# Kernel tuning notes

Hardware: AMD Instinct MI355X
Metric: run time of the kernel (lower is better)

## Reference

```python
import jax, jax.numpy as jnp
import numpy as np

N_NODES = 50000
N_EDGES = 100000
NUM_RELS = 200
IN_DIM = 64
OUT_DIM = 64


def setup_inputs() -> dict:
    key = jax.random.key(0)
    k1, k2, k3, k4, k5, k6 = jax.random.split(key, 6)
    input_h = jax.random.normal(k1, (N_NODES, IN_DIM), dtype=jnp.float32)
    src = jax.random.randint(k2, (N_EDGES,), 0, N_NODES, dtype=jnp.int32)
    rel = jax.random.randint(k3, (N_EDGES,), 0, NUM_RELS, dtype=jnp.int32)
    dst = jax.random.randint(k4, (N_EDGES,), 0, N_NODES, dtype=jnp.int32)
    edges = jnp.stack([src, rel, dst], axis=1)  # (E, 3)
    # xavier_normal for relation weight: std = sqrt(2/(in+out))
    w_std = float(np.sqrt(2.0 / (IN_DIM + OUT_DIM)))
    weight = jax.random.normal(k5, (NUM_RELS, IN_DIM, OUT_DIM), dtype=jnp.float32) * w_std
    # xavier_uniform with leaky_relu(0.2) gain for self-loop weight
    gain = float(np.sqrt(2.0 / (1.0 + 0.2 ** 2)))
    bound = gain * float(np.sqrt(6.0 / (IN_DIM + OUT_DIM)))
    self_loop_weight = jax.random.uniform(
        k6, (IN_DIM, OUT_DIM), dtype=jnp.float32, minval=-bound, maxval=bound)
    return {"input_h": input_h, "edges": edges, "weight": weight,
            "self_loop_weight": self_loop_weight}


def reference(input_h, edges, weight, self_loop_weight):
    src, rel, dst = edges[:, 0], edges[:, 1], edges[:, 2]
    num_nodes = input_h.shape[0]
    num_edges = edges.shape[0]

    src_h = input_h[src]                      # (E, in) gather
    w_e = weight[rel]                         # (E, in, out) per-edge weight materialization
    msg = jnp.einsum('ei,eio->eo', src_h, w_e)  # per-edge bmm

    # torch quirk: index_matrix[dst] = arange(E) keeps the LAST write per dst,
    # so each edge's message is replaced by the message of the last edge
    # (in edge order) with the same destination.
    last_idx = jax.ops.segment_max(jnp.arange(num_edges, dtype=jnp.int32), dst,
                                   num_segments=num_nodes)  # (N,)
    msg = msg[last_idx[dst]]                  # (E, out)

    # scatter-mean aggregation by destination (nodes with no in-edges get 0)
    msg_sum = jax.ops.segment_sum(msg, dst, num_segments=num_nodes)          # (N, out)
    count = jax.ops.segment_sum(jnp.ones((num_edges,), msg.dtype), dst,
                                num_segments=num_nodes)                      # (N,)
    agg = jnp.where(count[:, None] > 0, msg_sum / jnp.maximum(count, 1.0)[:, None], 0.0)

    out = input_h @ self_loop_weight + agg    # self-loop plus aggregated messages
    return out
```

## Files before the change

kernel.cpp:

```cpp
#include <hip/hip_runtime.h>

#define N_NODES 50000
#define N_EDGES 100000
#define NUM_RELS 200
#define DIM 64
#define CAP 512
#define TILES 8
#define HPAD 68

#define OFF_LAST 0
#define OFF_CUR  50000
#define OFF_BN   50200
#define OFF_BS   (50200 + NUM_RELS * CAP)

#define BUCKET_BLKS 196
#define SELF_BLKS   782

__global__ void init_kernel(int* __restrict__ ws) {
    int i = blockIdx.x * 256 + threadIdx.x;
    if (i < N_NODES) ws[OFF_LAST + i] = -1;
    if (i < NUM_RELS) ws[OFF_CUR + i] = 0;
}

__global__ void edge_max_kernel(const int* __restrict__ edges, int* __restrict__ ws) {
    int e = blockIdx.x * 256 + threadIdx.x;
    if (e < N_EDGES) atomicMax(&ws[OFF_LAST + edges[e * 3 + 2]], e);
}

__device__ __forceinline__ void gemm44(const float* __restrict__ Hl,
                                       const float* __restrict__ Wl,
                                       int e4, int c4, float acc[4][4]) {
#pragma unroll 8
    for (int k = 0; k < DIM; ++k) {
        float4 hv = *(const float4*)&Hl[k * HPAD + e4 * 4];
        float4 wv = *(const float4*)&Wl[k * DIM + c4 * 4];
        float hvv[4] = {hv.x, hv.y, hv.z, hv.w};
        float wvv[4] = {wv.x, wv.y, wv.z, wv.w};
#pragma unroll
        for (int i = 0; i < 4; ++i)
#pragma unroll
            for (int j = 0; j < 4; ++j)
                acc[i][j] = fmaf(hvv[i], wvv[j], acc[i][j]);
    }
}

__global__ __launch_bounds__(256) void bucket_self_kernel(
    const float* __restrict__ h,
    const int* __restrict__ edges,
    const float* __restrict__ wself,
    int* __restrict__ ws,
    float* __restrict__ out)
{
    __shared__ float Wl[DIM * DIM];
    __shared__ float Hl[DIM * HPAD];

    if (blockIdx.x < BUCKET_BLKS) {
        int n = blockIdx.x * 256 + threadIdx.x;
        if (n < N_NODES) {
            int li = ws[OFF_LAST + n];
            if (li >= 0) {
                int r = edges[li * 3 + 1];
                int s = edges[li * 3 + 0];
                int pos = atomicAdd(&ws[OFF_CUR + r], 1);
                if (pos < CAP) {
                    ws[OFF_BN + r * CAP + pos] = n;
                    ws[OFF_BS + r * CAP + pos] = s;
                }
            }
        }
        return;
    }

    int tile = blockIdx.x - BUCKET_BLKS;
    int base = tile * 64;
    int t = threadIdx.x;

    {
        const float4* wg = (const float4*)wself;
        float4* wl4 = (float4*)Wl;
#pragma unroll
        for (int j = 0; j < 4; ++j) wl4[t + j * 256] = wg[t + j * 256];
    }
    {
        int e = t & 63, q = t >> 6;
        int n = base + e; if (n >= N_NODES) n = N_NODES - 1;
        const float* hp = h + (size_t)n * DIM + q * 16;
#pragma unroll
        for (int j = 0; j < 4; ++j) {
            float4 v = *(const float4*)(hp + j * 4);
            int k0 = q * 16 + j * 4;
            Hl[(k0 + 0) * HPAD + e] = v.x;
            Hl[(k0 + 1) * HPAD + e] = v.y;
            Hl[(k0 + 2) * HPAD + e] = v.z;
            Hl[(k0 + 3) * HPAD + e] = v.w;
        }
    }
    __syncthreads();

    int c4 = t & 15, e4 = t >> 4;
    float acc[4][4];
#pragma unroll
    for (int i = 0; i < 4; ++i)
#pragma unroll
        for (int j = 0; j < 4; ++j) acc[i][j] = 0.f;

    gemm44(Hl, Wl, e4, c4, acc);

#pragma unroll
    for (int i = 0; i < 4; ++i) {
        int n = base + e4 * 4 + i;
        if (n < N_NODES)
            *(float4*)(out + (size_t)n * DIM + c4 * 4) =
                make_float4(acc[i][0], acc[i][1], acc[i][2], acc[i][3]);
    }
}

__global__ __launch_bounds__(256) void msg_kernel(const float* __restrict__ h,
                                                  const float* __restrict__ weight,
                                                  const int* __restrict__ ws,
                                                  float* __restrict__ out) {
    __shared__ float Wl[DIM * DIM];
    __shared__ float Hl[DIM * HPAD];

    int rel  = blockIdx.x >> 3;
    int tile = blockIdx.x & 7;
    int c = ws[OFF_CUR + rel];
    if (c > CAP) c = CAP;
    int start = tile * 64;
    if (start >= c) return;

    int t = threadIdx.x;
    const int* bn = ws + OFF_BN + rel * CAP;
    const int* bs = ws + OFF_BS + rel * CAP;

    {
        const float4* wg = (const float4*)(weight + (size_t)rel * DIM * DIM);
        float4* wl4 = (float4*)Wl;
#pragma unroll
        for (int j = 0; j < 4; ++j) wl4[t + j * 256] = wg[t + j * 256];
    }
    {
        int e = t & 63, q = t >> 6;
        int pos = start + e; if (pos >= c) pos = c - 1;
        int s = bs[pos];
        const float* hp = h + (size_t)s * DIM + q * 16;
#pragma unroll
        for (int j = 0; j < 4; ++j) {
            float4 v = *(const float4*)(hp + j * 4);
            int k0 = q * 16 + j * 4;
            Hl[(k0 + 0) * HPAD + e] = v.x;
            Hl[(k0 + 1) * HPAD + e] = v.y;
            Hl[(k0 + 2) * HPAD + e] = v.z;
            Hl[(k0 + 3) * HPAD + e] = v.w;
        }
    }
    __syncthreads();

    int c4 = t & 15, e4 = t >> 4;
    float acc[4][4];
#pragma unroll
    for (int i = 0; i < 4; ++i)
#pragma unroll
        for (int j = 0; j < 4; ++j) acc[i][j] = 0.f;

    gemm44(Hl, Wl, e4, c4, acc);

#pragma unroll
    for (int i = 0; i < 4; ++i) {
        int pos = start + e4 * 4 + i;
        if (pos < c) {
            int n = bn[pos];
            float* op = out + (size_t)n * DIM + c4 * 4;
            float4 cur = *(const float4*)op;
            *(float4*)op = make_float4(cur.x + acc[i][0], cur.y + acc[i][1],
                                       cur.z + acc[i][2], cur.w + acc[i][3]);
        }
    }
}

extern "C" void kernel_launch(void* const* d_in, const int* in_sizes, int n_in,
                              void* d_out, int out_size, void* d_ws, size_t ws_size,
                              hipStream_t stream) {
    const float* h      = (const float*)d_in[0];
    const int*   edges  = (const int*)d_in[1];
    const float* weight = (const float*)d_in[2];
    const float* wself  = (const float*)d_in[3];
    float* out = (float*)d_out;
    int* ws = (int*)d_ws;

    init_kernel<<<(N_NODES + 255) / 256, 256, 0, stream>>>(ws);
    edge_max_kernel<<<(N_EDGES + 255) / 256, 256, 0, stream>>>(edges, ws);
    bucket_self_kernel<<<BUCKET_BLKS + SELF_BLKS, 256, 0, stream>>>(h, edges, wself, ws, out);
    msg_kernel<<<NUM_RELS * TILES, 256, 0, stream>>>(h, weight, ws, out);
}
```

Measured before the change: 68.78 us.

## Convert inputs to bf16 and use MFMA for self-loop and message GEMMs

Adds a prep kernel that converts node features and relation and self-loop weights to bf16, with the weights transposed, and folds workspace initialization into the same launch. The self-loop and per-relation message GEMMs now use bf16 MFMA 16x16x32 instructions instead of scalar FP32 FMA register tiles. This is meant to cut gather bandwidth and ALU time in exchange for an extra conversion pass over all of h and the weights, plus reduced precision. Outputs are written as scalar stores per lane rather than float4.

After: 59.78 us. 13.1% less time.

```diff
diff --git a/kernel.cpp b/kernel.cpp
--- a/kernel.cpp
+++ b/kernel.cpp
@@ -6,20 +6,74 @@
 #define DIM 64
 #define CAP 512
 #define TILES 8
-#define HPAD 68
+#define KPAD 72
+
+typedef __attribute__((ext_vector_type(8))) short bf16x8;
+typedef __attribute__((ext_vector_type(8))) unsigned short u16x8;
+typedef __attribute__((ext_vector_type(4))) float f32x4;
 
 #define OFF_LAST 0
 #define OFF_CUR  50000
 #define OFF_BN   50200
-#define OFF_BS   (50200 + NUM_RELS * CAP)
-
-#define BUCKET_BLKS 196
-#define SELF_BLKS   782
-
-__global__ void init_kernel(int* __restrict__ ws) {
-    int i = blockIdx.x * 256 + threadIdx.x;
-    if (i < N_NODES) ws[OFF_LAST + i] = -1;
-    if (i < NUM_RELS) ws[OFF_CUR + i] = 0;
+#define OFF_BS   152600
+#define HB_OFF   1020032u
+#define WT_OFF   7420032u
+
+__device__ __forceinline__ unsigned short f2bf(float x) {
+    union { float f; unsigned u; } v; v.f = x;
+    unsigned r = v.u + 0x7FFFu + ((v.u >> 16) & 1u);
+    return (unsigned short)(r >> 16);
+}
+
+#define PREP_INIT 197
+#define PREP_WT   201
+#define PREP_HB   782
+
+__global__ __launch_bounds__(256) void prep_kernel(
+    const float* __restrict__ h, const float* __restrict__ weight,
+    const float* __restrict__ wself, int* __restrict__ ws,
+    unsigned short* __restrict__ hb, unsigned short* __restrict__ wt)
+{
+    __shared__ float Wl[DIM * DIM];
+    int b = blockIdx.x, t = threadIdx.x;
+
+    if (b < PREP_INIT) {
+        int i = b * 256 + t;
+        if (i < N_NODES) ws[OFF_LAST + i] = -1;
+        if (i < NUM_RELS) ws[OFF_CUR + i] = 0;
+        return;
+    }
+    if (b < PREP_INIT + PREP_WT) {
+        int rel = b - PREP_INIT;
+        const float* src = (rel < NUM_RELS) ? (weight + (size_t)rel * DIM * DIM) : wself;
+#pragma unroll
+        for (int j = 0; j < 16; ++j) Wl[t + j * 256] = src[t + j * 256];
+        __syncthreads();
+        int c = t >> 2, q = t & 3;
+        unsigned short tmp[16];
+#pragma unroll
+        for (int kk = 0; kk < 16; ++kk)
+            tmp[kk] = f2bf(Wl[(q * 16 + kk) * DIM + c]);
+        unsigned short* dst = wt + (size_t)rel * DIM * DIM + c * DIM + q * 16;
+        *(u16x8*)dst       = *(const u16x8*)&tmp[0];
+        *(u16x8*)(dst + 8) = *(const u16x8*)&tmp[8];
+        return;
+    }
+    {
+        long off = (long)(b - PREP_INIT - PREP_WT) * 4096 + (long)t * 16;
+        if (off < (long)N_NODES * DIM) {
+            const float4* src = (const float4*)(h + off);
+            unsigned short tmp[16];
+#pragma unroll
+            for (int j = 0; j < 4; ++j) {
+                float4 v = src[j];
+                tmp[j*4+0]=f2bf(v.x); tmp[j*4+1]=f2bf(v.y);
+                tmp[j*4+2]=f2bf(v.z); tmp[j*4+3]=f2bf(v.w);
+            }
+            *(u16x8*)(hb + off)     = *(const u16x8*)&tmp[0];
+            *(u16x8*)(hb + off + 8) = *(const u16x8*)&tmp[8];
+        }
+    }
 }
 
 __global__ void edge_max_kernel(const int* __restrict__ edges, int* __restrict__ ws) {
@@ -27,35 +81,20 @@
     if (e < N_EDGES) atomicMax(&ws[OFF_LAST + edges[e * 3 + 2]], e);
 }
 
-__device__ __forceinline__ void gemm44(const float* __restrict__ Hl,
-                                       const float* __restrict__ Wl,
-                                       int e4, int c4, float acc[4][4]) {
-#pragma unroll 8
-    for (int k = 0; k < DIM; ++k) {
-        float4 hv = *(const float4*)&Hl[k * HPAD + e4 * 4];
-        float4 wv = *(const float4*)&Wl[k * DIM + c4 * 4];
-        float hvv[4] = {hv.x, hv.y, hv.z, hv.w};
-        float wvv[4] = {wv.x, wv.y, wv.z, wv.w};
-#pragma unroll
-        for (int i = 0; i < 4; ++i)
-#pragma unroll
-            for (int j = 0; j < 4; ++j)
-                acc[i][j] = fmaf(hvv[i], wvv[j], acc[i][j]);
-    }
-}
+#define BUCKET_BLKS 196
+#define NODE_TILES 782
 
 __global__ __launch_bounds__(256) void bucket_self_kernel(
-    const float* __restrict__ h,
-    const int* __restrict__ edges,
-    const float* __restrict__ wself,
-    int* __restrict__ ws,
+    const int* __restrict__ edges, const unsigned short* __restrict__ hb,
+    const unsigned short* __restrict__ wt, int* __restrict__ ws,
     float* __restrict__ out)
 {
-    __shared__ float Wl[DIM * DIM];
-    __shared__ float Hl[DIM * HPAD];
+    __shared__ unsigned short Wsh[DIM * KPAD];
+    __shared__ unsigned short Hs[DIM * KPAD];
+    int t = threadIdx.x;
 
     if (blockIdx.x < BUCKET_BLKS) {
-        int n = blockIdx.x * 256 + threadIdx.x;
+        int n = blockIdx.x * 256 + t;
         if (n < N_NODES) {
             int li = ws[OFF_LAST + n];
             if (li >= 0) {
@@ -71,58 +110,54 @@
         return;
     }
 
-    int tile = blockIdx.x - BUCKET_BLKS;
-    int base = tile * 64;
-    int t = threadIdx.x;
-
+    int base = (blockIdx.x - BUCKET_BLKS) * 64;
+    int row = t >> 2, q = t & 3;
     {
-        const float4* wg = (const float4*)wself;
-        float4* wl4 = (float4*)Wl;
-#pragma unroll
-        for (int j = 0; j < 4; ++j) wl4[t + j * 256] = wg[t + j * 256];
-    }
-    {
-        int e = t & 63, q = t >> 6;
-        int n = base + e; if (n >= N_NODES) n = N_NODES - 1;
-        const float* hp = h + (size_t)n * DIM + q * 16;
-#pragma unroll
-        for (int j = 0; j < 4; ++j) {
-            float4 v = *(const float4*)(hp + j * 4);
-            int k0 = q * 16 + j * 4;
-            Hl[(k0 + 0) * HPAD + e] = v.x;
-            Hl[(k0 + 1) * HPAD + e] = v.y;
-            Hl[(k0 + 2) * HPAD + e] = v.z;
-            Hl[(k0 + 3) * HPAD + e] = v.w;
-        }
+        const unsigned short* wsrc = wt + (size_t)NUM_RELS * DIM * DIM + row * DIM + q * 16;
+        *(u16x8*)&Wsh[row * KPAD + q * 16]     = *(const u16x8*)wsrc;
+        *(u16x8*)&Wsh[row * KPAD + q * 16 + 8] = *(const u16x8*)(wsrc + 8);
+        int n = base + row; if (n >= N_NODES) n = N_NODES - 1;
+        const unsigned short* hsrc = hb + (size_t)n * DIM + q * 16;
+        *(u16x8*)&Hs[row * KPAD + q * 16]     = *(const u16x8*)hsrc;
+        *(u16x8*)&Hs[row * KPAD + q * 16 + 8] = *(const u16x8*)(hsrc + 8);
     }
     __syncthreads();
 
-    int c4 = t & 15, e4 = t >> 4;
-    float acc[4][4];
-#pragma unroll
-    for (int i = 0; i < 4; ++i)
-#pragma unroll
-        for (int j = 0; j < 4; ++j) acc[i][j] = 0.f;
-
-    gemm44(Hl, Wl, e4, c4, acc);
-
-#pragma unroll
-    for (int i = 0; i < 4; ++i) {
-        int n = base + e4 * 4 + i;
-        if (n < N_NODES)
-            *(float4*)(out + (size_t)n * DIM + c4 * 4) =
-                make_float4(acc[i][0], acc[i][1], acc[i][2], acc[i][3]);
-    }
-}
-
-__global__ __launch_bounds__(256) void msg_kernel(const float* __restrict__ h,
-                                                  const float* __restrict__ weight,
-                                                  const int* __restrict__ ws,
-                                                  float* __restrict__ out) {
-    __shared__ float Wl[DIM * DIM];
-    __shared__ float Hl[DIM * HPAD];
-
-    int rel  = blockIdx.x >> 3;
+    int l = t & 63;
+    int w = __builtin_amdgcn_readfirstlane(t >> 6);
+    int r16 = l & 15, kb = l >> 4;
+
+    bf16x8 a0 = *reinterpret_cast<const bf16x8*>(&Hs[(w * 16 + r16) * KPAD + kb * 8]);
+    bf16x8 a1 = *reinterpret_cast<const bf16x8*>(&Hs[(w * 16 + r16) * KPAD + 32 + kb * 8]);
+
+    int nn[4]; bool vv[4];
+#pragma unroll
+    for (int r = 0; r < 4; ++r) {
+        nn[r] = base + w * 16 + kb * 4 + r;
+        vv[r] = nn[r] < N_NODES;
+    }
+
+#pragma unroll
+    for (int n4 = 0; n4 < 4; ++n4) {
+        bf16x8 b0 = *reinterpret_cast<const bf16x8*>(&Wsh[(n4 * 16 + r16) * KPAD + kb * 8]);
+        bf16x8 b1 = *reinterpret_cast<const bf16x8*>(&Wsh[(n4 * 16 + r16) * KPAD + 32 + kb * 8]);
+        f32x4 acc = {0.f, 0.f, 0.f, 0.f};
+        acc = __builtin_amdgcn_mfma_f32_16x16x32_bf16(a0, b0, acc, 0, 0, 0);
+        acc = __builtin_amdgcn_mfma_f32_16x16x32_bf16(a1, b1, acc, 0, 0, 0);
+#pragma unroll
+        for (int r = 0; r < 4; ++r)
+            if (vv[r]) out[(size_t)nn[r] * DIM + n4 * 16 + r16] = acc[r];
+    }
+}
+
+__global__ __launch_bounds__(256) void msg_kernel(
+    const unsigned short* __restrict__ hb, const unsigned short* __restrict__ wt,
+    const int* __restrict__ ws, float* __restrict__ out)
+{
+    __shared__ unsigned short Wsh[DIM * KPAD];
+    __shared__ unsigned short Hs[DIM * KPAD];
+
+    int rel = blockIdx.x >> 3;
     int tile = blockIdx.x & 7;
     int c = ws[OFF_CUR + rel];
     if (c > CAP) c = CAP;
@@ -133,48 +168,44 @@
     const int* bn = ws + OFF_BN + rel * CAP;
     const int* bs = ws + OFF_BS + rel * CAP;
 
+    int row = t >> 2, q = t & 3;
     {
-        const float4* wg = (const float4*)(weight + (size_t)rel * DIM * DIM);
-        float4* wl4 = (float4*)Wl;
-#pragma unroll
-        for (int j = 0; j < 4; ++j) wl4[t + j * 256] = wg[t + j * 256];
-    }
-    {
-        int e = t & 63, q = t >> 6;
-        int pos = start + e; if (pos >= c) pos = c - 1;
+        const unsigned short* wsrc = wt + (size_t)rel * DIM * DIM + row * DIM + q * 16;
+        *(u16x8*)&Wsh[row * KPAD + q * 16]     = *(const u16x8*)wsrc;
+        *(u16x8*)&Wsh[row * KPAD + q * 16 + 8] = *(const u16x8*)(wsrc + 8);
+        int pos = start + row; if (pos >= c) pos = c - 1;
         int s = bs[pos];
-        const float* hp = h + (size_t)s * DIM + q * 16;
-#pragma unroll
-        for (int j = 0; j < 4; ++j) {
-            float4 v = *(const float4*)(hp + j * 4);
-            int k0 = q * 16 + j * 4;
-            Hl[(k0 + 0) * HPAD + e] = v.x;
-            Hl[(k0 + 1) * HPAD + e] = v.y;
-            Hl[(k0 + 2) * HPAD + e] = v.z;
-            Hl[(k0 + 3) * HPAD + e] = v.w;
-        }
+        const unsigned short* hsrc = hb + (size_t)s * DIM + q * 16;
+        *(u16x8*)&Hs[row * KPAD + q * 16]     = *(const u16x8*)hsrc;
+        *(u16x8*)&Hs[row * KPAD + q * 16 + 8] = *(const u16x8*)(hsrc + 8);
     }
     __syncthreads();
 
-    int c4 = t & 15, e4 = t >> 4;
-    float acc[4][4];
-#pragma unroll
-    for (int i = 0; i < 4; ++i)
-#pragma unroll
-        for (int j = 0; j < 4; ++j) acc[i][j] = 0.f;
-
-    gemm44(Hl, Wl, e4, c4, acc);
-
-#pragma unroll
-    for (int i = 0; i < 4; ++i) {
-        int pos = start + e4 * 4 + i;
-        if (pos < c) {
-            int n = bn[pos];
-            float* op = out + (size_t)n * DIM + c4 * 4;
-            float4 cur = *(const float4*)op;
-            *(float4*)op = make_float4(cur.x + acc[i][0], cur.y + acc[i][1],
-                                       cur.z + acc[i][2], cur.w + acc[i][3]);
-        }
+    int l = t & 63;
+    int w = __builtin_amdgcn_readfirstlane(t >> 6);
+    int r16 = l & 15, kb = l >> 4;
+
+    bf16x8 a0 = *reinterpret_cast<const bf16x8*>(&Hs[(w * 16 + r16) * KPAD + kb * 8]);
+    bf16x8 a1 = *reinterpret_cast<const bf16x8*>(&Hs[(w * 16 + r16) * KPAD + 32 + kb * 8]);
+
+    int nn[4]; bool vv[4];
+#pragma unroll
+    for (int r = 0; r < 4; ++r) {
+        int p = start + w * 16 + kb * 4 + r;
+        vv[r] = p < c;
+        nn[r] = bn[vv[r] ? p : 0];
+    }
+
+#pragma unroll
+    for (int n4 = 0; n4 < 4; ++n4) {
+        bf16x8 b0 = *reinterpret_cast<const bf16x8*>(&Wsh[(n4 * 16 + r16) * KPAD + kb * 8]);
+        bf16x8 b1 = *reinterpret_cast<const bf16x8*>(&Wsh[(n4 * 16 + r16) * KPAD + 32 + kb * 8]);
+        f32x4 acc = {0.f, 0.f, 0.f, 0.f};
+        acc = __builtin_amdgcn_mfma_f32_16x16x32_bf16(a0, b0, acc, 0, 0, 0);
+        acc = __builtin_amdgcn_mfma_f32_16x16x32_bf16(a1, b1, acc, 0, 0, 0);
+#pragma unroll
+        for (int r = 0; r < 4; ++r)
+            if (vv[r]) out[(size_t)nn[r] * DIM + n4 * 16 + r16] += acc[r];
     }
 }
 
@@ -186,10 +217,12 @@
     const float* weight = (const float*)d_in[2];
     const float* wself  = (const float*)d_in[3];
     float* out = (float*)d_out;
-    int* ws = (int*)d_ws;
-
-    init_kernel<<<(N_NODES + 255) / 256, 256, 0, stream>>>(ws);
-    edge_max_kernel<<<(N_EDGES + 255) / 256, 256, 0, stream>>>(edges, ws);
-    bucket_self_kernel<<<BUCKET_BLKS + SELF_BLKS, 256, 0, stream>>>(h, edges, wself, ws, out);
-    msg_kernel<<<NUM_RELS * TILES, 256, 0, stream>>>(h, weight, ws, out);
-}
+    int* wsi = (int*)d_ws;
+    unsigned short* hb = (unsigned short*)((char*)d_ws + HB_OFF);
+    unsigned short* wt = (unsigned short*)((char*)d_ws + WT_OFF);
+
+    prep_kernel<<<PREP_INIT + PREP_WT + PREP_HB, 256, 0, stream>>>(h, weight, wself, wsi, hb, wt);
+    edge_max_kernel<<<(N_EDGES + 255) / 256, 256, 0, stream>>>(edges, wsi);
+    bucket_self_kernel<<<BUCKET_BLKS + NODE_TILES, 256, 0, stream>>>(edges, hb, wt, wsi, out);
+    msg_kernel<<<NUM_RELS * TILES, 256, 0, stream>>>(hb, wt, wsi, out);
+}
```
